# Kernel optimization log

Hardware: AMD Instinct MI355X
Metric: run time of the kernel (lower is better)

Reference implementation:

```python
import jax, jax.numpy as jnp
import numpy as np
from jax import lax

DN = ('NHWC', 'HWIO', 'NHWC')  # conv dimension numbers


def setup_inputs() -> dict:
    key = jax.random.key(0)
    ks = jax.random.split(key, 10)
    B, H, W, C, F, E = 16, 32, 32, 128, 128, 8
    G = F * (H // 2) * (W // 2)  # 32768, gating flatten size
    return {
        'x': jax.random.normal(ks[0], (B, H, W, C), jnp.float32),
        'eps_kernel': jax.random.normal(ks[1], (3, 3, C, F, E), jnp.float32),
        'eps_gate': jax.random.normal(ks[2], (B, E), jnp.float32),
        'expert_mu': jax.random.normal(ks[3], (3, 3, C, F, E), jnp.float32) * 0.05,
        'expert_rho': jax.random.normal(ks[4], (3, C, F, E), jnp.float32) * 0.01 - 6.0,
        'expert_bias': jax.random.normal(ks[5], (F, E), jnp.float32) * 0.01,
        'gating_kernel': jax.random.normal(ks[6], (3, 3, C, F), jnp.float32) * 0.05,
        'gating_bias': jax.random.normal(ks[7], (F,), jnp.float32) * 0.01,
        'gating_out_kernel': jax.random.normal(ks[8], (G, E), jnp.float32) * 0.01,
        'gating_out_bias': jax.random.normal(ks[9], (E,), jnp.float32) * 0.01,
    }


def reference(x, eps_kernel, eps_gate, expert_mu, expert_rho, expert_bias,
              gating_kernel, gating_bias, gating_out_kernel, gating_out_bias):
    GATING_NOISE_SIGMA = 1e-4
    TOP_K = 2
    B = x.shape[0]
    kh, kw, C, F, E = expert_mu.shape

    # Bayesian reparameterized expert kernels: rho shared over first kernel dim
    sigma = jax.nn.softplus(expert_rho)[None]               # [1,kw,C,F,E]
    kernel = expert_mu + sigma * eps_kernel                 # [kh,kw,C,F,E]

    # All-expert conv as one grouped conv via output-channel packing
    kern_flat = kernel.reshape(kh, kw, C, F * E)
    expert_out = lax.conv_general_dilated(x, kern_flat, (1, 1), 'SAME',
                                          dimension_numbers=DN)
    expert_out = expert_out.reshape(B, x.shape[1], x.shape[2], F, E)
    expert_out = expert_out + expert_bias                   # [B,H,W,F,E]

    # Gating path: conv -> 2x2 maxpool -> flatten -> dense -> noisy logits
    g = lax.conv_general_dilated(x, gating_kernel, (1, 1), 'SAME',
                                 dimension_numbers=DN) + gating_bias
    g = lax.reduce_window(g, -jnp.inf, lax.max,
                          (1, 2, 2, 1), (1, 2, 2, 1), 'VALID')
    logits = g.reshape(B, -1) @ gating_out_kernel + gating_out_bias  # [B,E]
    logits = logits + GATING_NOISE_SIGMA * eps_gate

    # noisy top-k gating: softmax over selected experts, zero elsewhere
    top_vals, top_idx = lax.top_k(logits, TOP_K)
    top_w = jax.nn.softmax(top_vals, axis=-1)
    gates = jnp.zeros((B, E), logits.dtype).at[
        jnp.arange(B)[:, None], top_idx].set(top_w)

    # combine experts weighted by gates, broadcast over spatial dims
    out = jnp.einsum('bhwfe,be->bhwf', expert_out, gates)
    return out
```

## Files before the change

### kernel.cpp

```cpp
#include <hip/hip_runtime.h>
#include <cmath>

#define B_ 16
#define H_ 32
#define W_ 32
#define C_ 128
#define F_ 128
#define KSZ (9*C_*F_)
#define NKS 36
#define FRAG_ELE 4096

typedef __bf16 bf16;
typedef __bf16 bf16x4 __attribute__((ext_vector_type(4)));
typedef __bf16 bf16x8 __attribute__((ext_vector_type(8)));
typedef float  f32x4  __attribute__((ext_vector_type(4)));

__device__ __forceinline__ float softplus_f(float v) {
  return log1pf(expf(-fabsf(v))) + fmaxf(v, 0.f);
}

__device__ __forceinline__ float logit_f(const float* part, const float* gob,
                                         const float* epsg, int bb, int e) {
  float s = 0.f;
  #pragma unroll
  for (int hb = 0; hb < 16; ++hb) s += part[(bb*16 + hb)*8 + e];
  return s + gob[e] + 1e-4f * epsg[bb*8 + e];
}

__device__ __forceinline__ void block_map_f(int bid, int* b, int* hb) {
  *b  = (bid & 7) * 2 + (bid >> 7);
  *hb = (bid >> 3) & 15;
}

template<int MODE>
__global__ __launch_bounds__(1024, 4) void conv_k(
    const float* __restrict__ x,
    const bf16* __restrict__ Bhi,
    const bf16* __restrict__ Blo,
    const float* __restrict__ gb,
    const float* __restrict__ Wg,
    const float* __restrict__ part,
    const float* __restrict__ gob,
    const float* __restrict__ epsg,
    const float* __restrict__ ebias,
    const float* __restrict__ mu,
    const float* __restrict__ rho,
    const float* __restrict__ epsk,
    bf16* __restrict__ bank,
    float* __restrict__ outv)
{
  const int t   = threadIdx.x;
  const int l   = t & 63;

  if (MODE == 2 && blockIdx.x < NKS) {
    if (t < 512) {
      const int ks = blockIdx.x;
      const int nf = t >> 6;
      const int khkw = ks >> 2, kw = khkw % 3;
      const int f  = nf*16 + (l & 15);
      const int cb = (ks & 3)*32 + (l >> 4)*8;
      bf16x8 ob[8];
      #pragma unroll
      for (int j = 0; j < 8; ++j) {
        const int c = cb + j;
        const float* mp = &mu  [(size_t)((khkw*C_ + c)*F_ + f) * 8];
        const float* ep = &epsk[(size_t)((khkw*C_ + c)*F_ + f) * 8];
        const float* rp = &rho [(size_t)((kw  *C_ + c)*F_ + f) * 8];
        #pragma unroll
        for (int e = 0; e < 8; ++e)
          ob[e][j] = (bf16)(mp[e] + softplus_f(rp[e]) * ep[e]);
      }
      #pragma unroll
      for (int e = 0; e < 8; ++e) {
        size_t o = (size_t)e*KSZ + (size_t)ks*FRAG_ELE + nf*512 + l*8;
        *(bf16x8*)&bank[o] = ob[e];
      }
    }
    return;
  }

  int b, hb;
  block_map_f(MODE == 2 ? blockIdx.x - NKS : blockIdx.x, &b, &hb);
  const int wid = t >> 6;
  const int kg  = wid >> 3;
  const int w8  = wid & 7;

  __shared__ bf16 xs[MODE*4*34*128];
  __shared__ float red[8][8];
  __shared__ float gl8[8];
  __shared__ float gw2[2];
  __shared__ int   eid2[2];

  for (int v = t; v < 4*34*32; v += 1024) {
    int c4   = v & 31;
    int col  = (v >> 5) % 34;
    int rowi = (v >> 5) / 34;
    int row  = hb*2 - 1 + rowi;
    int w    = col - 1;
    float4 xv = make_float4(0.f, 0.f, 0.f, 0.f);
    if (row >= 0 && row < H_ && w >= 0 && w < W_)
      xv = *(const float4*)&x[((b*H_ + row)*W_ + w)*C_ + c4*4];
    float vv[4] = {xv.x, xv.y, xv.z, xv.w};
    bf16x4 h4, l4;
    #pragma unroll
    for (int j = 0; j < 4; ++j) {
      h4[j] = (bf16)vv[j];
      if (MODE == 2) l4[j] = (bf16)(vv[j] - (float)h4[j]);
    }
    int base = ((rowi*34 + col)*256 + c4*8) ^ ((col & 7) << 4);
    *(bf16x4*)((char*)xs + base) = h4;
    if (MODE == 2) *(bf16x4*)((char*)xs + 34816 + base) = l4;
  }
  if (MODE == 1 && t == 0) {
    float lg[8];
    #pragma unroll
    for (int e = 0; e < 8; ++e) lg[e] = logit_f(part, gob, epsg, b, e);
    int i0 = 0;
    #pragma unroll
    for (int e = 1; e < 8; ++e) if (lg[e] > lg[i0]) i0 = e;
    int i1 = (i0 == 0) ? 1 : 0;
    #pragma unroll
    for (int e = 0; e < 8; ++e) if (e != i0 && lg[e] > lg[i1]) i1 = e;
    float m  = fmaxf(lg[i0], lg[i1]);
    float e0 = expf(lg[i0] - m), e1 = expf(lg[i1] - m);
    float s  = e0 + e1;
    #pragma unroll
    for (int e = 0; e < 8; ++e) gl8[e] = 0.f;
    gl8[i0] = e0 / s;  gl8[i1] = e1 / s;
    eid2[0] = i0;      eid2[1] = i1;
    gw2[0]  = e0 / s;  gw2[1]  = e1 / s;
  }
  __syncthreads();

  const int mpar = w8 & 1;
  const int nf0  = (w8 >> 1) << 1;
  const int r15  = l & 15;
  const int q    = l >> 4;

  f32x4 acc00 = {0.f,0.f,0.f,0.f}, acc01 = acc00, acc10 = acc00, acc11 = acc00;
  f32x4 acd00 = acc00, acd01 = acc00, acd10 = acc00, acd11 = acc00;

  const bf16* B0;
  const bf16* B1;
  if (MODE == 1) { B0 = Bhi + (size_t)eid2[0]*KSZ; B1 = Bhi + (size_t)eid2[1]*KSZ; }
  else           { B0 = Bhi;                       B1 = Blo; }
  const size_t bgo = (size_t)(nf0*512 + l*8);

  bf16x8 s0h0,s0h1,s0l0,s0l1, s1h0,s1h1,s1l0,s1l1, s2h0,s2h1,s2l0,s2l1;

#define LOADB(S, KS_) do {                                                  \
    int kk_ = (KS_); if (kk_ > NKS-1) kk_ = NKS-1;                          \
    size_t o_ = bgo + (size_t)kk_ * FRAG_ELE;                               \
    S##h0 = *(const bf16x8*)(B0 + o_);                                      \
    S##h1 = *(const bf16x8*)(B0 + o_ + 512);                                \
    S##l0 = *(const bf16x8*)(B1 + o_);                                      \
    S##l1 = *(const bf16x8*)(B1 + o_ + 512);                                \
  } while (0)

#define MFMA16(a, bb_, c) __builtin_amdgcn_mfma_f32_16x16x32_bf16(a, bb_, c, 0, 0, 0)

#define COMPUTE(S, KS_) do {                                                \
    const int khkw_ = (KS_) >> 2;                                           \
    const int kh_ = khkw_ / 3, kw_ = khkw_ % 3;                             \
    const int c0_ = ((KS_) & 3) << 5;                                       \
    const int col_ = mpar*16 + r15 + kw_;                                   \
    const int off_ = ((kh_*34 + col_)*256 + (c0_ + q*8)*2) ^ ((col_ & 7) << 4); \
    bf16x8 a0_ = *(const bf16x8*)((const char*)xs + off_);                  \
    bf16x8 a1_ = *(const bf16x8*)((const char*)xs + off_ + 8704);           \
    __builtin_amdgcn_s_setprio(1);                                          \
    acc00 = MFMA16(a0_, S##h0, acc00);                                      \
    acc01 = MFMA16(a0_, S##h1, acc01);                                      \
    acc10 = MFMA16(a1_, S##h0, acc10);                                      \
    acc11 = MFMA16(a1_, S##h1, acc11);                                      \
    if (MODE == 2) {                                                        \
      bf16x8 g0_ = *(const bf16x8*)((const char*)xs + 34816 + off_);        \
      bf16x8 g1_ = *(const bf16x8*)((const char*)xs + 34816 + off_ + 8704); \
      acc00 = MFMA16(g0_, S##h0, acc00);                                    \
      acc01 = MFMA16(g0_, S##h1, acc01);                                    \
      acc10 = MFMA16(g1_, S##h0, acc10);                                    \
      acc11 = MFMA16(g1_, S##h1, acc11);                                    \
      acc00 = MFMA16(a0_, S##l0, acc00);                                    \
      acc01 = MFMA16(a0_, S##l1, acc01);                                    \
      acc10 = MFMA16(a1_, S##l0, acc10);                                    \
      acc11 = MFMA16(a1_, S##l1, acc11);                                    \
    } else {                                                                \
      acd00 = MFMA16(a0_, S##l0, acd00);                                    \
      acd01 = MFMA16(a0_, S##l1, acd01);                                    \
      acd10 = MFMA16(a1_, S##l0, acd10);                                    \
      acd11 = MFMA16(a1_, S##l1, acd11);                                    \
    }                                                                       \
    __builtin_amdgcn_s_setprio(0);                                          \
  } while (0)

  const int ks0 = kg * (NKS/2);
  LOADB(s0, ks0); LOADB(s1, ks0+1); LOADB(s2, ks0+2);
  for (int ks = ks0; ks < ks0 + NKS/2; ks += 3) {
    COMPUTE(s0, ks);   LOADB(s0, ks+3);
    COMPUTE(s1, ks+1); LOADB(s1, ks+4);
    COMPUTE(s2, ks+2); LOADB(s2, ks+5);
  }
#undef LOADB
#undef COMPUTE

  if (MODE == 1) {
    const float g0 = gw2[0], g1 = gw2[1];
    #pragma unroll
    for (int r = 0; r < 4; ++r) {
      acc00[r] = g0*acc00[r] + g1*acd00[r];
      acc01[r] = g0*acc01[r] + g1*acd01[r];
      acc10[r] = g0*acc10[r] + g1*acd10[r];
      acc11[r] = g0*acc11[r] + g1*acd11[r];
    }
  }

  __syncthreads();
  float* comb = (float*)xs;
  if (kg == 1) {
    #pragma unroll
    for (int r = 0; r < 4; ++r) {
      comb[(w8*16 + 0  + r)*64 + l] = acc00[r];
      comb[(w8*16 + 4  + r)*64 + l] = acc01[r];
      comb[(w8*16 + 8  + r)*64 + l] = acc10[r];
      comb[(w8*16 + 12 + r)*64 + l] = acc11[r];
    }
  }
  __syncthreads();
  if (kg == 0) {
    #pragma unroll
    for (int r = 0; r < 4; ++r) {
      acc00[r] += comb[(w8*16 + 0  + r)*64 + l];
      acc01[r] += comb[(w8*16 + 4  + r)*64 + l];
      acc10[r] += comb[(w8*16 + 8  + r)*64 + l];
      acc11[r] += comb[(w8*16 + 12 + r)*64 + l];
    }
  }

  if (MODE == 1) {
    if (kg == 0) {
      const int f0 = nf0*16 + r15;
      float bv0 = 0.f, bv1 = 0.f;
      #pragma unroll
      for (int e = 0; e < 8; ++e) {
        bv0 += gl8[e] * ebias[f0*8 + e];
        bv1 += gl8[e] * ebias[(f0+16)*8 + e];
      }
      #pragma unroll
      for (int mi = 0; mi < 2; ++mi) {
        const int h = hb*2 + mi;
        #pragma unroll
        for (int r = 0; r < 4; ++r) {
          const int wo = mpar*16 + q*4 + r;
          float* o = &outv[((b*H_ + h)*W_ + wo)*F_];
          o[f0]      = (mi ? acc10[r] : acc00[r]) + bv0;
          o[f0 + 16] = (mi ? acc11[r] : acc01[r]) + bv1;
        }
      }
    }
  } else {
    float pr[8] = {0,0,0,0,0,0,0,0};
    if (kg == 0) {
      #pragma unroll
      for (int ni = 0; ni < 2; ++ni) {
        const int f = (nf0 + ni)*16 + r15;
        const float bv = gb[f];
        #pragma unroll
        for (int pp = 0; pp < 2; ++pp) {
          float m0 = ni ? fmaxf(acc01[2*pp], acc01[2*pp+1])
                        : fmaxf(acc00[2*pp], acc00[2*pp+1]);
          float m1 = ni ? fmaxf(acc11[2*pp], acc11[2*pp+1])
                        : fmaxf(acc10[2*pp], acc10[2*pp+1]);
          float pm = fmaxf(m0, m1) + bv;
          const int pw = mpar*8 + q*2 + pp;
          const float* wr = &Wg[(size_t)((hb*16 + pw)*128 + f) * 8];
          float4 wA = *(const float4*)wr;
          float4 wB = *(const float4*)(wr + 4);
          pr[0] += pm*wA.x; pr[1] += pm*wA.y; pr[2] += pm*wA.z; pr[3] += pm*wA.w;
          pr[4] += pm*wB.x; pr[5] += pm*wB.y; pr[6] += pm*wB.z; pr[7] += pm*wB.w;
        }
      }
    }
    #pragma unroll
    for (int o = 32; o > 0; o >>= 1)
      #pragma unroll
      for (int e = 0; e < 8; ++e) pr[e] += __shfl_down(pr[e], o);
    if (l == 0 && kg == 0)
      #pragma unroll
      for (int e = 0; e < 8; ++e) red[w8][e] = pr[e];
    __syncthreads();
    if (t < 8) {
      float s = 0.f;
      #pragma unroll
      for (int w = 0; w < 8; ++w) s += red[w][t];
      outv[(b*16 + hb)*8 + t] = s;
    }
  }
}

__global__ __launch_bounds__(1024) void gkprep_k(
    const float* __restrict__ gk, bf16* __restrict__ bgh, bf16* __restrict__ bgl)
{
  __shared__ float tile[32*129];
  const int ks   = blockIdx.x;
  const int khkw = ks >> 2;
  const int cb   = (ks & 3)*32;
  const int t    = threadIdx.x;

  {
    int c  = t >> 5;
    int f4 = (t & 31) * 4;
    float4 val = *(const float4*)&gk[(size_t)(khkw*C_ + cb + c)*F_ + f4];
    float* dst = &tile[c*129 + f4];
    dst[0] = val.x; dst[1] = val.y; dst[2] = val.z; dst[3] = val.w;
  }
  __syncthreads();

  if (t < 512) {
    const int nf = t >> 6, l = t & 63;
    const int f  = nf*16 + (l & 15);
    bf16x8 h8, l8;
    #pragma unroll
    for (int j = 0; j < 8; ++j) {
      int c = (l >> 4)*8 + j;
      float v = tile[c*129 + f];
      bf16 h = (bf16)v;
      h8[j] = h;
      l8[j] = (bf16)(v - (float)h);
    }
    *(bf16x8*)&bgh[(size_t)ks*FRAG_ELE + t*8] = h8;
    *(bf16x8*)&bgl[(size_t)ks*FRAG_ELE + t*8] = l8;
  }
}

extern "C" void kernel_launch(void* const* d_in, const int* in_sizes, int n_in,
                              void* d_out, int out_size, void* d_ws, size_t ws_size,
                              hipStream_t stream) {
  const float* x    = (const float*)d_in[0];
  const float* epsk = (const float*)d_in[1];
  const float* epsg = (const float*)d_in[2];
  const float* mu   = (const float*)d_in[3];
  const float* rho  = (const float*)d_in[4];
  const float* ebias= (const float*)d_in[5];
  const float* gk   = (const float*)d_in[6];
  const float* gb   = (const float*)d_in[7];
  const float* gok  = (const float*)d_in[8];
  const float* gob  = (const float*)d_in[9];
  float* out = (float*)d_out;

  char* ws = (char*)d_ws;
  bf16*  bank = (bf16*) (ws);
  bf16*  bgh  = (bf16*) (ws + 2359296);
  bf16*  bgl  = (bf16*) (ws + 2654208);
  float* part = (float*)(ws + 2949120);

  gkprep_k<<<NKS, 1024, 0, stream>>>(gk, bgh, bgl);
  conv_k<2><<<NKS + 256, 1024, 0, stream>>>(x, bgh, bgl, gb, gok,
                                            nullptr, nullptr, nullptr, nullptr,
                                            mu, rho, epsk, bank, part);
  conv_k<1><<<256, 1024, 0, stream>>>(x, bank, nullptr, nullptr, nullptr,
                                      part, gob, epsg, ebias,
                                      nullptr, nullptr, nullptr, nullptr, out);
}
```

Measured before the change: 54.85 us.

## Use single-bf16 gating conv with 3xbf16 fallback for close top-k margins

The gating conv now runs in plain bf16 (one MFMA pass instead of three split-precision passes). A new fix kernel checks each batch's gap between its second and third logits. Only when that gap is below a threshold does it recompute the gating partials with the hi/lo split precision. The expert-kernel bank construction moves into this fix kernel. This adds a kernel launch and a data-dependent branch, and it relies on the threshold being wide enough that bf16 error never flips the top-k selection.

```diff
diff --git a/kernel.cpp b/kernel.cpp
--- a/kernel.cpp
+++ b/kernel.cpp
@@ -9,6 +9,7 @@
 #define KSZ (9*C_*F_)
 #define NKS 36
 #define FRAG_ELE 4096
+#define TAU 0.05f
 
 typedef __bf16 bf16;
 typedef __bf16 bf16x4 __attribute__((ext_vector_type(4)));
@@ -27,6 +28,22 @@
   return s + gob[e] + 1e-4f * epsg[bb*8 + e];
 }
 
+__device__ __forceinline__ void top3_f(const float* lg, int* o0, int* o1,
+                                       float* gap) {
+  int i0 = 0;
+  #pragma unroll
+  for (int e = 1; e < 8; ++e) if (lg[e] > lg[i0]) i0 = e;
+  int i1 = (i0 == 0) ? 1 : 0;
+  #pragma unroll
+  for (int e = 0; e < 8; ++e) if (e != i0 && lg[e] > lg[i1]) i1 = e;
+  int i2 = 0;
+  while (i2 == i0 || i2 == i1) ++i2;
+  #pragma unroll
+  for (int e = 0; e < 8; ++e)
+    if (e != i0 && e != i1 && lg[e] > lg[i2]) i2 = e;
+  *o0 = i0; *o1 = i1; *gap = lg[i1] - lg[i2];
+}
+
 __device__ __forceinline__ void block_map_f(int bid, int* b, int* hb) {
   *b  = (bid & 7) * 2 + (bid >> 7);
   *hb = (bid >> 3) & 15;
@@ -35,57 +52,25 @@
 template<int MODE>
 __global__ __launch_bounds__(1024, 4) void conv_k(
     const float* __restrict__ x,
-    const bf16* __restrict__ Bhi,
-    const bf16* __restrict__ Blo,
+    const bf16* __restrict__ Bbank,
     const float* __restrict__ gb,
     const float* __restrict__ Wg,
     const float* __restrict__ part,
+    const float* __restrict__ part2,
     const float* __restrict__ gob,
     const float* __restrict__ epsg,
     const float* __restrict__ ebias,
-    const float* __restrict__ mu,
-    const float* __restrict__ rho,
-    const float* __restrict__ epsk,
-    bf16* __restrict__ bank,
     float* __restrict__ outv)
 {
+  int b, hb;
+  block_map_f(blockIdx.x, &b, &hb);
   const int t   = threadIdx.x;
   const int l   = t & 63;
-
-  if (MODE == 2 && blockIdx.x < NKS) {
-    if (t < 512) {
-      const int ks = blockIdx.x;
-      const int nf = t >> 6;
-      const int khkw = ks >> 2, kw = khkw % 3;
-      const int f  = nf*16 + (l & 15);
-      const int cb = (ks & 3)*32 + (l >> 4)*8;
-      bf16x8 ob[8];
-      #pragma unroll
-      for (int j = 0; j < 8; ++j) {
-        const int c = cb + j;
-        const float* mp = &mu  [(size_t)((khkw*C_ + c)*F_ + f) * 8];
-        const float* ep = &epsk[(size_t)((khkw*C_ + c)*F_ + f) * 8];
-        const float* rp = &rho [(size_t)((kw  *C_ + c)*F_ + f) * 8];
-        #pragma unroll
-        for (int e = 0; e < 8; ++e)
-          ob[e][j] = (bf16)(mp[e] + softplus_f(rp[e]) * ep[e]);
-      }
-      #pragma unroll
-      for (int e = 0; e < 8; ++e) {
-        size_t o = (size_t)e*KSZ + (size_t)ks*FRAG_ELE + nf*512 + l*8;
-        *(bf16x8*)&bank[o] = ob[e];
-      }
-    }
-    return;
-  }
-
-  int b, hb;
-  block_map_f(MODE == 2 ? blockIdx.x - NKS : blockIdx.x, &b, &hb);
   const int wid = t >> 6;
   const int kg  = wid >> 3;
   const int w8  = wid & 7;
 
-  __shared__ bf16 xs[MODE*4*34*128];
+  __shared__ bf16 xs[4*34*128];
   __shared__ float red[8][8];
   __shared__ float gl8[8];
   __shared__ float gw2[2];
@@ -100,27 +85,23 @@
     float4 xv = make_float4(0.f, 0.f, 0.f, 0.f);
     if (row >= 0 && row < H_ && w >= 0 && w < W_)
       xv = *(const float4*)&x[((b*H_ + row)*W_ + w)*C_ + c4*4];
-    float vv[4] = {xv.x, xv.y, xv.z, xv.w};
-    bf16x4 h4, l4;
-    #pragma unroll
-    for (int j = 0; j < 4; ++j) {
-      h4[j] = (bf16)vv[j];
-      if (MODE == 2) l4[j] = (bf16)(vv[j] - (float)h4[j]);
-    }
+    bf16x4 h4;
+    h4[0] = (bf16)xv.x; h4[1] = (bf16)xv.y;
+    h4[2] = (bf16)xv.z; h4[3] = (bf16)xv.w;
     int base = ((rowi*34 + col)*256 + c4*8) ^ ((col & 7) << 4);
     *(bf16x4*)((char*)xs + base) = h4;
-    if (MODE == 2) *(bf16x4*)((char*)xs + 34816 + base) = l4;
   }
   if (MODE == 1 && t == 0) {
     float lg[8];
     #pragma unroll
     for (int e = 0; e < 8; ++e) lg[e] = logit_f(part, gob, epsg, b, e);
-    int i0 = 0;
-    #pragma unroll
-    for (int e = 1; e < 8; ++e) if (lg[e] > lg[i0]) i0 = e;
-    int i1 = (i0 == 0) ? 1 : 0;
-    #pragma unroll
-    for (int e = 0; e < 8; ++e) if (e != i0 && lg[e] > lg[i1]) i1 = e;
+    int i0, i1; float gap;
+    top3_f(lg, &i0, &i1, &gap);
+    if (gap < TAU) {
+      #pragma unroll
+      for (int e = 0; e < 8; ++e) lg[e] = logit_f(part2, gob, epsg, b, e);
+      top3_f(lg, &i0, &i1, &gap);
+    }
     float m  = fmaxf(lg[i0], lg[i1]);
     float e0 = expf(lg[i0] - m), e1 = expf(lg[i1] - m);
     float s  = e0 + e1;
@@ -142,8 +123,8 @@
 
   const bf16* B0;
   const bf16* B1;
-  if (MODE == 1) { B0 = Bhi + (size_t)eid2[0]*KSZ; B1 = Bhi + (size_t)eid2[1]*KSZ; }
-  else           { B0 = Bhi;                       B1 = Blo; }
+  if (MODE == 1) { B0 = Bbank + (size_t)eid2[0]*KSZ; B1 = Bbank + (size_t)eid2[1]*KSZ; }
+  else           { B0 = Bbank;                       B1 = Bbank; }
   const size_t bgo = (size_t)(nf0*512 + l*8);
 
   bf16x8 s0h0,s0h1,s0l0,s0l1, s1h0,s1h1,s1l0,s1l1, s2h0,s2h1,s2l0,s2l1;
@@ -153,8 +134,10 @@
     size_t o_ = bgo + (size_t)kk_ * FRAG_ELE;                               \
     S##h0 = *(const bf16x8*)(B0 + o_);                                      \
     S##h1 = *(const bf16x8*)(B0 + o_ + 512);                                \
-    S##l0 = *(const bf16x8*)(B1 + o_);                                      \
-    S##l1 = *(const bf16x8*)(B1 + o_ + 512);                                \
+    if (MODE == 1) {                                                        \
+      S##l0 = *(const bf16x8*)(B1 + o_);                                    \
+      S##l1 = *(const bf16x8*)(B1 + o_ + 512);                              \
+    }                                                                       \
   } while (0)
 
 #define MFMA16(a, bb_, c) __builtin_amdgcn_mfma_f32_16x16x32_bf16(a, bb_, c, 0, 0, 0)
@@ -172,18 +155,7 @@
     acc01 = MFMA16(a0_, S##h1, acc01);                                      \
     acc10 = MFMA16(a1_, S##h0, acc10);                                      \
     acc11 = MFMA16(a1_, S##h1, acc11);                                      \
-    if (MODE == 2) {                                                        \
-      bf16x8 g0_ = *(const bf16x8*)((const char*)xs + 34816 + off_);        \
-      bf16x8 g1_ = *(const bf16x8*)((const char*)xs + 34816 + off_ + 8704); \
-      acc00 = MFMA16(g0_, S##h0, acc00);                                    \
-      acc01 = MFMA16(g0_, S##h1, acc01);                                    \
-      acc10 = MFMA16(g1_, S##h0, acc10);                                    \
-      acc11 = MFMA16(g1_, S##h1, acc11);                                    \
-      acc00 = MFMA16(a0_, S##l0, acc00);                                    \
-      acc01 = MFMA16(a0_, S##l1, acc01);                                    \
-      acc10 = MFMA16(a1_, S##l0, acc10);                                    \
-      acc11 = MFMA16(a1_, S##l1, acc11);                                    \
-    } else {                                                                \
+    if (MODE == 1) {                                                        \
       acd00 = MFMA16(a0_, S##l0, acd00);                                    \
       acd01 = MFMA16(a0_, S##l1, acd01);                                    \
       acd10 = MFMA16(a1_, S##l0, acd10);                                    \
@@ -296,6 +268,205 @@
   }
 }
 
+__global__ __launch_bounds__(1024, 4) void fix_k(
+    const float* __restrict__ x,
+    const bf16* __restrict__ bgh, const bf16* __restrict__ bgl,
+    const float* __restrict__ gb, const float* __restrict__ Wg,
+    const float* __restrict__ part, const float* __restrict__ gob,
+    const float* __restrict__ epsg,
+    const float* __restrict__ mu, const float* __restrict__ rho,
+    const float* __restrict__ epsk,
+    bf16* __restrict__ bank, float* __restrict__ part2)
+{
+  const int t = threadIdx.x;
+  const int l = t & 63;
+
+  if (blockIdx.x < NKS) {
+    if (t < 512) {
+      const int ks = blockIdx.x;
+      const int nf = t >> 6;
+      const int khkw = ks >> 2, kw = khkw % 3;
+      const int f  = nf*16 + (l & 15);
+      const int cb = (ks & 3)*32 + (l >> 4)*8;
+      bf16x8 ob[8];
+      #pragma unroll
+      for (int j = 0; j < 8; ++j) {
+        const int c = cb + j;
+        const float* mp = &mu  [(size_t)((khkw*C_ + c)*F_ + f) * 8];
+        const float* ep = &epsk[(size_t)((khkw*C_ + c)*F_ + f) * 8];
+        const float* rp = &rho [(size_t)((kw  *C_ + c)*F_ + f) * 8];
+        #pragma unroll
+        for (int e = 0; e < 8; ++e)
+          ob[e][j] = (bf16)(mp[e] + softplus_f(rp[e]) * ep[e]);
+      }
+      #pragma unroll
+      for (int e = 0; e < 8; ++e) {
+        size_t o = (size_t)e*KSZ + (size_t)ks*FRAG_ELE + nf*512 + l*8;
+        *(bf16x8*)&bank[o] = ob[e];
+      }
+    }
+    return;
+  }
+
+  int b, hb;
+  block_map_f(blockIdx.x - NKS, &b, &hb);
+  __shared__ int risky;
+  if (t == 0) {
+    float lg[8];
+    #pragma unroll
+    for (int e = 0; e < 8; ++e) lg[e] = logit_f(part, gob, epsg, b, e);
+    int i0, i1; float gap;
+    top3_f(lg, &i0, &i1, &gap);
+    risky = (gap < TAU) ? 1 : 0;
+  }
+  __syncthreads();
+  if (!risky) return;
+
+  __shared__ bf16 xs[2*4*34*128];
+  __shared__ float red[8][8];
+  const int wid = t >> 6;
+  const int kg  = wid >> 3;
+  const int w8  = wid & 7;
+
+  for (int v = t; v < 4*34*32; v += 1024) {
+    int c4   = v & 31;
+    int col  = (v >> 5) % 34;
+    int rowi = (v >> 5) / 34;
+    int row  = hb*2 - 1 + rowi;
+    int w    = col - 1;
+    float4 xv = make_float4(0.f, 0.f, 0.f, 0.f);
+    if (row >= 0 && row < H_ && w >= 0 && w < W_)
+      xv = *(const float4*)&x[((b*H_ + row)*W_ + w)*C_ + c4*4];
+    float vv[4] = {xv.x, xv.y, xv.z, xv.w};
+    bf16x4 h4, l4;
+    #pragma unroll
+    for (int j = 0; j < 4; ++j) {
+      h4[j] = (bf16)vv[j];
+      l4[j] = (bf16)(vv[j] - (float)h4[j]);
+    }
+    int base = ((rowi*34 + col)*256 + c4*8) ^ ((col & 7) << 4);
+    *(bf16x4*)((char*)xs + base) = h4;
+    *(bf16x4*)((char*)xs + 34816 + base) = l4;
+  }
+  __syncthreads();
+
+  const int mpar = w8 & 1;
+  const int nf0  = (w8 >> 1) << 1;
+  const int r15  = l & 15;
+  const int q    = l >> 4;
+
+  f32x4 acc00 = {0.f,0.f,0.f,0.f}, acc01 = acc00, acc10 = acc00, acc11 = acc00;
+  const size_t bgo = (size_t)(nf0*512 + l*8);
+  bf16x8 s0h0,s0h1,s0l0,s0l1, s1h0,s1h1,s1l0,s1l1, s2h0,s2h1,s2l0,s2l1;
+
+#define FLOADB(S, KS_) do {                                                 \
+    int kk_ = (KS_); if (kk_ > NKS-1) kk_ = NKS-1;                          \
+    size_t o_ = bgo + (size_t)kk_ * FRAG_ELE;                               \
+    S##h0 = *(const bf16x8*)(bgh + o_);                                     \
+    S##h1 = *(const bf16x8*)(bgh + o_ + 512);                               \
+    S##l0 = *(const bf16x8*)(bgl + o_);                                     \
+    S##l1 = *(const bf16x8*)(bgl + o_ + 512);                               \
+  } while (0)
+
+#define MFMA16(a, bb_, c) __builtin_amdgcn_mfma_f32_16x16x32_bf16(a, bb_, c, 0, 0, 0)
+
+#define FCOMPUTE(S, KS_) do {                                               \
+    const int khkw_ = (KS_) >> 2;                                           \
+    const int kh_ = khkw_ / 3, kw_ = khkw_ % 3;                             \
+    const int c0_ = ((KS_) & 3) << 5;                                       \
+    const int col_ = mpar*16 + r15 + kw_;                                   \
+    const int off_ = ((kh_*34 + col_)*256 + (c0_ + q*8)*2) ^ ((col_ & 7) << 4); \
+    bf16x8 a0_ = *(const bf16x8*)((const char*)xs + off_);                  \
+    bf16x8 a1_ = *(const bf16x8*)((const char*)xs + off_ + 8704);           \
+    bf16x8 g0_ = *(const bf16x8*)((const char*)xs + 34816 + off_);          \
+    bf16x8 g1_ = *(const bf16x8*)((const char*)xs + 34816 + off_ + 8704);   \
+    __builtin_amdgcn_s_setprio(1);                                          \
+    acc00 = MFMA16(a0_, S##h0, acc00);                                      \
+    acc01 = MFMA16(a0_, S##h1, acc01);                                      \
+    acc10 = MFMA16(a1_, S##h0, acc10);                                      \
+    acc11 = MFMA16(a1_, S##h1, acc11);                                      \
+    acc00 = MFMA16(g0_, S##h0, acc00);                                      \
+    acc01 = MFMA16(g0_, S##h1, acc01);                                      \
+    acc10 = MFMA16(g1_, S##h0, acc10);                                      \
+    acc11 = MFMA16(g1_, S##h1, acc11);                                      \
+    acc00 = MFMA16(a0_, S##l0, acc00);                                      \
+    acc01 = MFMA16(a0_, S##l1, acc01);                                      \
+    acc10 = MFMA16(a1_, S##l0, acc10);                                      \
+    acc11 = MFMA16(a1_, S##l1, acc11);                                      \
+    __builtin_amdgcn_s_setprio(0);                                          \
+  } while (0)
+
+  const int ks0 = kg * (NKS/2);
+  FLOADB(s0, ks0); FLOADB(s1, ks0+1); FLOADB(s2, ks0+2);
+  for (int ks = ks0; ks < ks0 + NKS/2; ks += 3) {
+    FCOMPUTE(s0, ks);   FLOADB(s0, ks+3);
+    FCOMPUTE(s1, ks+1); FLOADB(s1, ks+4);
+    FCOMPUTE(s2, ks+2); FLOADB(s2, ks+5);
+  }
+#undef FLOADB
+#undef FCOMPUTE
+#undef MFMA16
+
+  __syncthreads();
+  float* comb = (float*)xs;
+  if (kg == 1) {
+    #pragma unroll
+    for (int r = 0; r < 4; ++r) {
+      comb[(w8*16 + 0  + r)*64 + l] = acc00[r];
+      comb[(w8*16 + 4  + r)*64 + l] = acc01[r];
+      comb[(w8*16 + 8  + r)*64 + l] = acc10[r];
+      comb[(w8*16 + 12 + r)*64 + l] = acc11[r];
+    }
+  }
+  __syncthreads();
+  if (kg == 0) {
+    #pragma unroll
+    for (int r = 0; r < 4; ++r) {
+      acc00[r] += comb[(w8*16 + 0  + r)*64 + l];
+      acc01[r] += comb[(w8*16 + 4  + r)*64 + l];
+      acc10[r] += comb[(w8*16 + 8  + r)*64 + l];
+      acc11[r] += comb[(w8*16 + 12 + r)*64 + l];
+    }
+  }
+
+  float pr[8] = {0,0,0,0,0,0,0,0};
+  if (kg == 0) {
+    #pragma unroll
+    for (int ni = 0; ni < 2; ++ni) {
+      const int f = (nf0 + ni)*16 + r15;
+      const float bv = gb[f];
+      #pragma unroll
+      for (int pp = 0; pp < 2; ++pp) {
+        float m0 = ni ? fmaxf(acc01[2*pp], acc01[2*pp+1])
+                      : fmaxf(acc00[2*pp], acc00[2*pp+1]);
+        float m1 = ni ? fmaxf(acc11[2*pp], acc11[2*pp+1])
+                      : fmaxf(acc10[2*pp], acc10[2*pp+1]);
+        float pm = fmaxf(m0, m1) + bv;
+        const int pw = mpar*8 + q*2 + pp;
+        const float* wr = &Wg[(size_t)((hb*16 + pw)*128 + f) * 8];
+        float4 wA = *(const float4*)wr;
+        float4 wB = *(const float4*)(wr + 4);
+        pr[0] += pm*wA.x; pr[1] += pm*wA.y; pr[2] += pm*wA.z; pr[3] += pm*wA.w;
+        pr[4] += pm*wB.x; pr[5] += pm*wB.y; pr[6] += pm*wB.z; pr[7] += pm*wB.w;
+      }
+    }
+  }
+  #pragma unroll
+  for (int o = 32; o > 0; o >>= 1)
+    #pragma unroll
+    for (int e = 0; e < 8; ++e) pr[e] += __shfl_down(pr[e], o);
+  if (l == 0 && kg == 0)
+    #pragma unroll
+    for (int e = 0; e < 8; ++e) red[w8][e] = pr[e];
+  __syncthreads();
+  if (t < 8) {
+    float s = 0.f;
+    #pragma unroll
+    for (int w = 0; w < 8; ++w) s += red[w][t];
+    part2[(b*16 + hb)*8 + t] = s;
+  }
+}
+
 __global__ __launch_bounds__(1024) void gkprep_k(
     const float* __restrict__ gk, bf16* __restrict__ bgh, bf16* __restrict__ bgl)
 {
@@ -347,16 +518,18 @@
   float* out = (float*)d_out;
 
   char* ws = (char*)d_ws;
-  bf16*  bank = (bf16*) (ws);
-  bf16*  bgh  = (bf16*) (ws + 2359296);
-  bf16*  bgl  = (bf16*) (ws + 2654208);
-  float* part = (float*)(ws + 2949120);
+  bf16*  bank  = (bf16*) (ws);
+  bf16*  bgh   = (bf16*) (ws + 2359296);
+  bf16*  bgl   = (bf16*) (ws + 2654208);
+  float* part  = (float*)(ws + 2949120);
+  float* part2 = (float*)(ws + 2957312);
 
   gkprep_k<<<NKS, 1024, 0, stream>>>(gk, bgh, bgl);
-  conv_k<2><<<NKS + 256, 1024, 0, stream>>>(x, bgh, bgl, gb, gok,
-                                            nullptr, nullptr, nullptr, nullptr,
-                                            mu, rho, epsk, bank, part);
-  conv_k<1><<<256, 1024, 0, stream>>>(x, bank, nullptr, nullptr, nullptr,
-                                      part, gob, epsg, ebias,
-                                      nullptr, nullptr, nullptr, nullptr, out);
-}
+  conv_k<2><<<256, 1024, 0, stream>>>(x, bgh, gb, gok,
+                                      nullptr, nullptr, nullptr, nullptr,
+                                      nullptr, part);
+  fix_k<<<NKS + 256, 1024, 0, stream>>>(x, bgh, bgl, gb, gok, part, gob,
+                                        epsg, mu, rho, epsk, bank, part2);
+  conv_k<1><<<256, 1024, 0, stream>>>(x, bank, nullptr, nullptr,
+                                      part, part2, gob, epsg, ebias, out);
+}
```

After: 60.55 us. +10.4%, slower.
